# Optimization experiments

Hardware: AMD Instinct MI355X
Metric: run time of the kernel (lower is better)

Reference implementation:

```python
import jax, jax.numpy as jnp
import numpy as np

# ---------------- geometry constants (from init_kwargs) ----------------
N_PROJ = 96          # cone-beam projections (batch of 2D BP, views of 3D BP)
A2D    = 96          # 2D parallel angles (= detector rows of cone sinogram)
DET2D  = 192         # 2D detector bins   (= detector cols of cone sinogram)
DS2D   = 1.0         # 2D detector spacing
H = 128
W = 128              # intermediate CB_projection image (geom_2d volume)
Zd = 128
Yd = 128
Xd = 128             # reconstruction volume (geometry.volume_shape)
DSO = 500.0          # source-isocenter distance
DSD = 1000.0         # source-detector distance
DU = 3.5
DV = 3.5             # 3D detector spacing (detector grid == H x W image grid)


def _grad_lastdim(x):
    # torch.gradient(x, dim=-1) with unit spacing: central diffs, one-sided edges
    left = x[..., 1:2] - x[..., 0:1]
    mid = (x[..., 2:] - x[..., :-2]) * 0.5
    right = x[..., -1:] - x[..., -2:-1]
    return jnp.concatenate([left, mid, right], axis=-1)


def _image_grid(h, w):
    ys = jnp.arange(h, dtype=jnp.float32) - (h - 1) / 2.0
    xs = jnp.arange(w, dtype=jnp.float32) - (w - 1) / 2.0
    yg, xg = jnp.meshgrid(ys, xs, indexing='ij')  # [h, w]
    return yg, xg


def _weights_3d():
    # Defrise-Clack intermediate-function weighting: cosine of ray angle,
    # w(x,y) = D / sqrt(D^2 + x^2 + y^2) on the intermediate image grid.
    yg, xg = _image_grid(H, W)
    return DSD / jnp.sqrt(DSD * DSD + xg * xg + yg * yg)


def _bp2d(sino):
    # Pixel-driven 2D parallel backprojection, batched over N.
    # sino: [N, A2D, DET2D] -> [N, H, W]
    yg, xg = _image_grid(H, W)
    th = jnp.arange(A2D, dtype=jnp.float32) * (np.pi / A2D)
    s = jnp.cos(th)[:, None, None] * xg + jnp.sin(th)[:, None, None] * yg  # [A,H,W]
    pos = s / DS2D + (DET2D - 1) / 2.0
    i0 = jnp.floor(pos).astype(jnp.int32)
    f = pos - i0
    i1 = i0 + 1
    w0 = jnp.where((i0 >= 0) & (i0 < DET2D), 1.0 - f, 0.0)
    w1 = jnp.where((i1 >= 0) & (i1 < DET2D), f, 0.0)
    i0c = jnp.clip(i0, 0, DET2D - 1)
    i1c = jnp.clip(i1, 0, DET2D - 1)
    aa = jnp.arange(A2D)[:, None, None]  # [A,1,1]
    g0 = sino[:, aa, i0c]  # [N, A, H, W]
    g1 = sino[:, aa, i1c]
    return (g0 * w0 + g1 * w1).sum(axis=1)  # [N, H, W]


def _bp3d(projs):
    # Voxel-driven circular cone-beam backprojection with FDK distance weight.
    # projs: [N_PROJ, H, W] (V=H rows, U=W cols) -> volume [Zd, Yd, Xd]
    zs = jnp.arange(Zd, dtype=jnp.float32) - (Zd - 1) / 2.0
    ys = jnp.arange(Yd, dtype=jnp.float32) - (Yd - 1) / 2.0
    xs = jnp.arange(Xd, dtype=jnp.float32) - (Xd - 1) / 2.0
    zz, yy, xx = jnp.meshgrid(zs, ys, xs, indexing='ij')  # [Z,Y,X]
    betas = jnp.arange(N_PROJ, dtype=jnp.float32) * (2.0 * np.pi / N_PROJ)

    def body(acc, inp):
        beta, proj = inp
        cb, sb = jnp.cos(beta), jnp.sin(beta)
        t = xx * cb + yy * sb          # along central ray
        s = -xx * sb + yy * cb         # transaxial offset
        r = DSO + t                    # source-to-voxel-plane distance
        pu = (DSD * s / r) / DU + (W - 1) / 2.0
        pv = (DSD * zz / r) / DV + (H - 1) / 2.0
        iu0 = jnp.floor(pu).astype(jnp.int32); fu = pu - iu0; iu1 = iu0 + 1
        iv0 = jnp.floor(pv).astype(jnp.int32); fv = pv - iv0; iv1 = iv0 + 1
        mu0 = (iu0 >= 0) & (iu0 < W); mu1 = (iu1 >= 0) & (iu1 < W)
        mv0 = (iv0 >= 0) & (iv0 < H); mv1 = (iv1 >= 0) & (iv1 < H)
        iu0c = jnp.clip(iu0, 0, W - 1); iu1c = jnp.clip(iu1, 0, W - 1)
        iv0c = jnp.clip(iv0, 0, H - 1); iv1c = jnp.clip(iv1, 0, H - 1)
        w00 = jnp.where(mv0 & mu0, (1 - fv) * (1 - fu), 0.0)
        w01 = jnp.where(mv0 & mu1, (1 - fv) * fu, 0.0)
        w10 = jnp.where(mv1 & mu0, fv * (1 - fu), 0.0)
        w11 = jnp.where(mv1 & mu1, fv * fu, 0.0)
        val = (proj[iv0c, iu0c] * w00 + proj[iv0c, iu1c] * w01 +
               proj[iv1c, iu0c] * w10 + proj[iv1c, iu1c] * w11)
        acc = acc + val * (DSD / r) ** 2
        return acc, None

    acc, _ = jax.lax.scan(body, jnp.zeros((Zd, Yd, Xd), jnp.float32), (betas, projs))
    return acc


def setup_inputs() -> dict:
    key = jax.random.key(0)
    k1, k2 = jax.random.split(key)
    sinogram = jax.random.normal(k1, (1, 1, N_PROJ, A2D, DET2D), dtype=jnp.float32)
    weight = jax.random.uniform(k2, (1, N_PROJ, A2D, DET2D), dtype=jnp.float32)
    prelu_weight = jnp.full((1,), 0.25, dtype=jnp.float32)
    return {"sinogram": sinogram, "weight": weight, "prelu_weight": prelu_weight}


def reference(sinogram, weight, prelu_weight):
    ws = sinogram[0] * weight                 # [1, N, A, D]
    deriv = _grad_lastdim(ws)[0]              # [N, A, D]  (squeeze dim 0)
    cb = _bp2d(deriv)                         # [N, H, W]
    weighted_cb = cb * _weights_3d()          # [N, H, W]
    reco = _bp3d(weighted_cb)[None]           # [1, Z, Y, X]
    a = prelu_weight[0]
    return jnp.where(reco >= 0, reco, a * reco)  # PReLU (single parameter)
```

## Files before the change

kernel.cpp:

```cpp
#include <hip/hip_runtime.h>
#include <hip/hip_fp16.h>
#include <math.h>

#define NPROJ 96
#define NANG  96
#define DET   192
#define NPIX  16384
#define SLICE (NANG*DET)

#define KPROJ 285.7142857142857f

__device__ __forceinline__ float frcp(float x) { return __builtin_amdgcn_rcpf(x); }

__device__ __forceinline__ float ffract(float x) {
#if __has_builtin(__builtin_amdgcn_fractf)
    return __builtin_amdgcn_fractf(x);
#else
    return x - floorf(x);
#endif
}

typedef __fp16 h2 __attribute__((ext_vector_type(2)));

__device__ __forceinline__ unsigned pack2(float a, float b) {
    h2 p = __builtin_amdgcn_cvt_pkrtz(a, b);
    return __builtin_bit_cast(unsigned, p);
}
__device__ __forceinline__ h2 as_h2(unsigned u) { return __builtin_bit_cast(h2, u); }

#if __has_builtin(__builtin_amdgcn_fdot2)
#define FDOT2(a, b, c) __builtin_amdgcn_fdot2((a), (b), (c), false)
#else
__device__ __forceinline__ float FDOT2(h2 a, h2 b, float c) {
    return c + (float)a[0] * (float)b[0] + (float)a[1] * (float)b[1];
}
#endif

__global__ __launch_bounds__(192) void k_deriv(const float* __restrict__ sino,
                                               const float* __restrict__ wgt,
                                               unsigned* __restrict__ derivp) {
    __shared__ float row[DET];
    const int r = blockIdx.x;
    const int d = threadIdx.x;
    const int base = r * DET + d;
    row[d] = sino[base] * wgt[base];
    __syncthreads();
    auto grad = [&](int i) -> float {
        i = (i > DET-1) ? DET-1 : i;
        if (i == 0)       return row[1] - row[0];
        if (i == DET-1)   return row[DET-1] - row[DET-2];
        return 0.5f * (row[i+1] - row[i-1]);
    };
    const float g0 = grad(d), g1 = grad(d+1);
    derivp[base] = pack2(g0, g1 - g0);
}

__global__ __launch_bounds__(256) void k_bp2d(const unsigned* __restrict__ derivp,
                                              unsigned* __restrict__ wq_dw) {
    __shared__ float sc[NANG], ss[NANG];
    __shared__ float buf[512];
    const int p   = blockIdx.x;
    const int tid = threadIdx.x;

    if (tid < NANG) {
        float s_, c_;
        sincosf((float)tid * (float)(3.14159265358979323846 / 96.0), &s_, &c_);
        sc[tid] = c_; ss[tid] = s_;
    }

    const int pixbase = blockIdx.y * 512;
    float acc[2], fx[2], fy[2];
    #pragma unroll
    for (int i = 0; i < 2; ++i) {
        const int pix = pixbase + i*256 + tid;
        fx[i] = (float)(pix & 127) - 63.5f;
        fy[i] = (float)(pix >> 7)  - 63.5f;
        acc[i] = 0.0f;
    }
    __syncthreads();

    const unsigned* rowp = derivp + p * SLICE;
    for (int a = 0; a < NANG; ++a, rowp += DET) {
        const float cb = sc[a], sb = ss[a];
        #pragma unroll
        for (int i = 0; i < 2; ++i) {
            const float pos = fmaf(cb, fx[i], fmaf(sb, fy[i], 95.5f));
            const int   i0  = (int)pos;
            const float f   = ffract(pos);
            acc[i] = FDOT2(as_h2(rowp[i0]), as_h2(pack2(1.0f, f)), acc[i]);
        }
    }

    #pragma unroll
    for (int i = 0; i < 2; ++i) {
        const float w = 1000.0f * rsqrtf(1000000.0f + fx[i]*fx[i] + fy[i]*fy[i]);
        buf[i*256 + tid] = acc[i] * w;
    }
    __syncthreads();

    unsigned* sq = wq_dw + p * (NPIX * 2);
    #pragma unroll
    for (int i = 0; i < 2; ++i) {
        const int l   = i*256 + tid;
        const int pix = pixbase + l;
        const int u   = pix & 127;
        const int v   = pix >> 7;
        const float v0 = buf[l];
        const float v1 = (u < 127) ? buf[l + 1] : 0.0f;
        const unsigned pr = pack2(v0, v1 - v0);
        sq[(((v << 7) + u) << 1)] = pr;
        if (v >= 1) sq[((((v - 1) << 7) + u) << 1) + 1] = pr;
    }
}

__global__ __launch_bounds__(256) void k_bp3d_p(const uint2* __restrict__ wp,
                                                const float* __restrict__ prelu,
                                                float* __restrict__ out) {
    __shared__ float sc[NPROJ], ss[NPROJ];
    const int tid = threadIdx.x;
    const int x   = tid & 127;
    const int y   = (blockIdx.x << 1) | (tid >> 7);
    const int z0  = blockIdx.y << 3;

    if (tid < NPROJ) {
        float s_, c_;
        sincosf((float)tid * (float)(2.0 * 3.14159265358979323846 / 96.0), &s_, &c_);
        sc[tid] = c_; ss[tid] = s_;
    }

    const float fx  = (float)x - 63.5f;
    const float fy  = (float)y - 63.5f;
    float za[4];
    #pragma unroll
    for (int j = 0; j < 4; ++j) za[j] = (float)z0 - 63.5f + (float)(2*j);

    float acc[8];
    #pragma unroll
    for (int j = 0; j < 8; ++j) acc[j] = 0.0f;

    __syncthreads();

    const char* bbc = (const char*)wp;
    for (int b = 0; b < NPROJ; ++b, bbc += (size_t)NPIX * sizeof(uint2)) {
        const float cb    = sc[b], sb = ss[b];
        const float t     = fmaf(fx, cb,  fy * sb);
        const float sdist = fmaf(fy, cb, -fx * sb);
        const float invr  = frcp(500.0f + t);
        const float pu    = fmaf(KPROJ * sdist, invr, 63.5f);
        const int   iu0   = (int)pu;
        const float fu    = ffract(pu);
        float w2 = 1000.0f * invr; w2 *= w2;
        const float Kz    = KPROJ * invr;
        const h2    wuw   = as_h2(pack2(w2, fu * w2));
        const unsigned ub = ((unsigned)iu0) << 3;

        #pragma unroll
        for (int pr2 = 0; pr2 < 4; ++pr2) {
            const float pvA = fmaf(Kz, za[pr2], 63.5f);
            const float pvB = pvA + Kz;
            const int   ivA = (int)pvA;
            const int   ivB = (int)pvB;
            const float fvA = ffract(pvA);
            const float fvB = ffract(pvB);
            const uint2 qA  = *(const uint2*)(bbc + ((((unsigned)ivA) << 10) + ub));
            const uint2 qB  = *(const uint2*)(bbc + ((((unsigned)ivB) << 10) + ub));
            const float tA  = FDOT2(as_h2(qA.x), wuw, 0.0f);
            const float bA  = FDOT2(as_h2(qA.y), wuw, 0.0f);
            acc[2*pr2]     += fmaf(fvA, bA - tA, tA);
            const float tB  = FDOT2(as_h2(qB.x), wuw, 0.0f);
            const float bB  = FDOT2(as_h2(qB.y), wuw, 0.0f);
            acc[2*pr2 + 1] += fmaf(fvB, bB - tB, tB);
        }
    }

    const float a = prelu[0];
    #pragma unroll
    for (int j = 0; j < 8; ++j) {
        const float v = acc[j];
        out[((z0 + j) << 14) + (y << 7) + x] = (v >= 0.0f) ? v : a * v;
    }
}

extern "C" void kernel_launch(void* const* d_in, const int* in_sizes, int n_in,
                              void* d_out, int out_size, void* d_ws, size_t ws_size,
                              hipStream_t stream) {
    const float* sino  = (const float*)d_in[0];
    const float* wgt   = (const float*)d_in[1];
    const float* prelu = (const float*)d_in[2];
    float* out = (float*)d_out;

    unsigned* wq_dw  = (unsigned*)d_ws;
    unsigned* derivp = wq_dw + (size_t)NPROJ * NPIX * 2;

    k_deriv<<<dim3(NPROJ * NANG), dim3(192), 0, stream>>>(sino, wgt, derivp);
    k_bp2d <<<dim3(NPROJ, 32),    dim3(256), 0, stream>>>(derivp, wq_dw);
    k_bp3d_p<<<dim3(64, 16),      dim3(256), 0, stream>>>((const uint2*)wq_dw, prelu, out);
}
```

Measured before the change: 212.0 us.

## Split projections across thread halves in 3D backprojection and use buffer loads

The 3D backprojection now gives each block a single y row. The two 128-thread halves each accumulate half of the projections for the same voxels, and the partial sums are combined through shared memory before the PReLU. This doubles the grid size for more latency hiding. Both gather loops switch to raw buffer-load intrinsics with a scalar offset, to reduce per-lane 64-bit address arithmetic. The cost is an extra shared-memory exchange and barrier at the end.

```diff
diff --git a/kernel.cpp b/kernel.cpp
--- a/kernel.cpp
+++ b/kernel.cpp
@@ -35,6 +35,22 @@
     return c + (float)a[0] * (float)b[0] + (float)a[1] * (float)b[1];
 }
 #endif
+
+typedef int v4i   __attribute__((ext_vector_type(4)));
+typedef unsigned u32x2 __attribute__((ext_vector_type(2)));
+
+extern "C" __device__ u32x2    llvm_buf_load_x2(v4i rsrc, int voffset, int soffset, int aux) __asm("llvm.amdgcn.raw.buffer.load.v2i32");
+extern "C" __device__ unsigned llvm_buf_load_x1(v4i rsrc, int voffset, int soffset, int aux) __asm("llvm.amdgcn.raw.buffer.load.i32");
+
+__device__ __forceinline__ v4i make_srsrc(const void* p, unsigned bytes) {
+    const unsigned long long a = (unsigned long long)p;
+    v4i r;
+    r.x = (int)(unsigned)(a & 0xffffffffull);
+    r.y = (int)(unsigned)(a >> 32);
+    r.z = (int)bytes;
+    r.w = 0x00020000;
+    return r;
+}
 
 __global__ __launch_bounds__(192) void k_deriv(const float* __restrict__ sino,
                                                const float* __restrict__ wgt,
@@ -79,15 +95,17 @@
     }
     __syncthreads();
 
-    const unsigned* rowp = derivp + p * SLICE;
-    for (int a = 0; a < NANG; ++a, rowp += DET) {
+    const v4i rsrc = make_srsrc(derivp, NPROJ * SLICE * 4u);
+    int soff = p * (SLICE * 4);
+    for (int a = 0; a < NANG; ++a, soff += DET * 4) {
         const float cb = sc[a], sb = ss[a];
         #pragma unroll
         for (int i = 0; i < 2; ++i) {
             const float pos = fmaf(cb, fx[i], fmaf(sb, fy[i], 95.5f));
             const int   i0  = (int)pos;
             const float f   = ffract(pos);
-            acc[i] = FDOT2(as_h2(rowp[i0]), as_h2(pack2(1.0f, f)), acc[i]);
+            const unsigned q = llvm_buf_load_x1(rsrc, i0 << 2, soff, 0);
+            acc[i] = FDOT2(as_h2(q), as_h2(pack2(1.0f, f)), acc[i]);
         }
     }
 
@@ -113,13 +131,15 @@
     }
 }
 
-__global__ __launch_bounds__(256) void k_bp3d_p(const uint2* __restrict__ wp,
+__global__ __launch_bounds__(256) void k_bp3d_s(const unsigned* __restrict__ wp_raw,
                                                 const float* __restrict__ prelu,
                                                 float* __restrict__ out) {
     __shared__ float sc[NPROJ], ss[NPROJ];
+    __shared__ float xch[2][4][128];
     const int tid = threadIdx.x;
     const int x   = tid & 127;
-    const int y   = (blockIdx.x << 1) | (tid >> 7);
+    const int g   = tid >> 7;
+    const int y   = blockIdx.x;
     const int z0  = blockIdx.y << 3;
 
     if (tid < NPROJ) {
@@ -130,9 +150,7 @@
 
     const float fx  = (float)x - 63.5f;
     const float fy  = (float)y - 63.5f;
-    float za[4];
-    #pragma unroll
-    for (int j = 0; j < 4; ++j) za[j] = (float)z0 - 63.5f + (float)(2*j);
+    const float zlo = (float)z0 - 63.5f;
 
     float acc[8];
     #pragma unroll
@@ -140,9 +158,11 @@
 
     __syncthreads();
 
-    const char* bbc = (const char*)wp;
-    for (int b = 0; b < NPROJ; ++b, bbc += (size_t)NPIX * sizeof(uint2)) {
-        const float cb    = sc[b], sb = ss[b];
+    const v4i rsrc = make_srsrc(wp_raw, NPROJ * NPIX * 8u);
+    int soff = g * (48 * NPIX * 8);
+    const int btrig0 = g * 48;
+    for (int b = 0; b < 48; ++b, soff += NPIX * 8) {
+        const float cb    = sc[btrig0 + b], sb = ss[btrig0 + b];
         const float t     = fmaf(fx, cb,  fy * sb);
         const float sdist = fmaf(fy, cb, -fx * sb);
         const float invr  = frcp(500.0f + t);
@@ -152,18 +172,18 @@
         float w2 = 1000.0f * invr; w2 *= w2;
         const float Kz    = KPROJ * invr;
         const h2    wuw   = as_h2(pack2(w2, fu * w2));
-        const unsigned ub = ((unsigned)iu0) << 3;
+        const int   ub    = iu0 << 3;
 
         #pragma unroll
         for (int pr2 = 0; pr2 < 4; ++pr2) {
-            const float pvA = fmaf(Kz, za[pr2], 63.5f);
+            const float pvA = fmaf(Kz, zlo + (float)(2*pr2), 63.5f);
             const float pvB = pvA + Kz;
             const int   ivA = (int)pvA;
             const int   ivB = (int)pvB;
             const float fvA = ffract(pvA);
             const float fvB = ffract(pvB);
-            const uint2 qA  = *(const uint2*)(bbc + ((((unsigned)ivA) << 10) + ub));
-            const uint2 qB  = *(const uint2*)(bbc + ((((unsigned)ivB) << 10) + ub));
+            const u32x2 qA  = llvm_buf_load_x2(rsrc, (ivA << 10) + ub, soff, 0);
+            const u32x2 qB  = llvm_buf_load_x2(rsrc, (ivB << 10) + ub, soff, 0);
             const float tA  = FDOT2(as_h2(qA.x), wuw, 0.0f);
             const float bA  = FDOT2(as_h2(qA.y), wuw, 0.0f);
             acc[2*pr2]     += fmaf(fvA, bA - tA, tA);
@@ -173,11 +193,16 @@
         }
     }
 
+    #pragma unroll
+    for (int j = 0; j < 4; ++j) xch[g][j][x] = acc[4*(1 - g) + j];
+    __syncthreads();
+
     const float a = prelu[0];
     #pragma unroll
-    for (int j = 0; j < 8; ++j) {
-        const float v = acc[j];
-        out[((z0 + j) << 14) + (y << 7) + x] = (v >= 0.0f) ? v : a * v;
+    for (int j = 0; j < 4; ++j) {
+        const int   jz = 4*g + j;
+        const float v  = acc[jz] + xch[1 - g][j][x];
+        out[((z0 + jz) << 14) + (y << 7) + x] = (v >= 0.0f) ? v : a * v;
     }
 }
 
@@ -192,7 +217,7 @@
     unsigned* wq_dw  = (unsigned*)d_ws;
     unsigned* derivp = wq_dw + (size_t)NPROJ * NPIX * 2;
 
-    k_deriv<<<dim3(NPROJ * NANG), dim3(192), 0, stream>>>(sino, wgt, derivp);
-    k_bp2d <<<dim3(NPROJ, 32),    dim3(256), 0, stream>>>(derivp, wq_dw);
-    k_bp3d_p<<<dim3(64, 16),      dim3(256), 0, stream>>>((const uint2*)wq_dw, prelu, out);
-}
+    k_deriv <<<dim3(NPROJ * NANG), dim3(192), 0, stream>>>(sino, wgt, derivp);
+    k_bp2d  <<<dim3(NPROJ, 32),    dim3(256), 0, stream>>>(derivp, wq_dw);
+    k_bp3d_s<<<dim3(128, 16),      dim3(256), 0, stream>>>(wq_dw, prelu, out);
+}
```

Result: faster. 205.9 us (-2.9%).
